# Kernel tuning notes

Measured on AMD Instinct MI355X. Metric: run time of the kernel, lower is better.

The kernel has to match this reference:

```python
import jax, jax.numpy as jnp
import numpy as np

N1 = 200000          # total nodes in batched data1
B = 8                # graphs in data1 (equal-sized)
NPG = N1 // B        # nodes per graph = 25000
N2 = 199             # total nodes in data2 (forced by fc1 in_features 9950 = 50*199)
K = 50               # SortAggregation k
E1 = 2000000
E2 = 3184
F_IN = 128
LN_EPS = 1e-5


def _lin(x, W, b):
    return x @ W + b


def _gin(x, ei, W1a, b1a, W1b, b1b, W2a, b2a, W2b, b2b):
    # GINConv with eps=0: nn((1+eps)*x + sum_{j in N(i)} x_j); messages flow ei[0] -> ei[1]
    agg = jnp.zeros_like(x).at[ei[1]].add(x[ei[0]])
    h = _lin(jax.nn.relu(_lin(x + agg, W1a, b1a)), W1b, b1b)
    h = jax.nn.relu(h)
    agg = jnp.zeros_like(h).at[ei[1]].add(h[ei[0]])
    h2 = _lin(jax.nn.relu(_lin(h + agg, W2a, b2a)), W2b, b2b)
    return jax.nn.relu(h2)


def _cdist(a, b):
    # torch.cdist p=2: [N1, D] x [N2, D] -> [N1, N2]
    sq = (a * a).sum(-1, keepdims=True) + (b * b).sum(-1)[None, :] - 2.0 * (a @ b.T)
    return jnp.sqrt(jnp.maximum(sq, 0.0))


def _sort_pool(x_dense, k):
    # DGCNN sort pooling: sort nodes per graph by last channel, descending; take top-k
    # x_dense: [B, N, D] (all graphs full, so no fill-value padding needed)
    order = jnp.argsort(-x_dense[:, :, -1], axis=-1)[:, :k]       # [B, k]
    return jnp.take_along_axis(x_dense, order[:, :, None], axis=1)  # [B, k, D]


def _layernorm(x, g, b):
    mu = x.mean(-1, keepdims=True)
    var = ((x - mu) ** 2).mean(-1, keepdims=True)
    return (x - mu) * jax.lax.rsqrt(var + LN_EPS) * g + b


def setup_inputs() -> dict:
    key = jax.random.key(0)
    ks = jax.random.split(key, 32)
    s = 0.05
    inp = {
        "x1": jax.random.normal(ks[0], (N1, F_IN), jnp.float32),
        "edge_index1": jax.random.randint(ks[1], (2, E1), 0, N1, jnp.int64),
        "batch1": jnp.repeat(jnp.arange(B, dtype=jnp.int64), NPG),
        "x2": jax.random.normal(ks[2], (N2, F_IN), jnp.float32),
        "edge_index2": jax.random.randint(ks[3], (2, E2), 0, N2, jnp.int64),
        # GIN conv1 MLP: Linear(128,128), ReLU, Linear(128,128)
        "W1a": jax.random.normal(ks[4], (F_IN, 128), jnp.float32) * s,
        "b1a": jnp.zeros((128,), jnp.float32),
        "W1b": jax.random.normal(ks[5], (128, 128), jnp.float32) * s,
        "b1b": jnp.zeros((128,), jnp.float32),
        # GIN conv2 MLP: Linear(128,64), ReLU, Linear(64,64)
        "W2a": jax.random.normal(ks[6], (128, 64), jnp.float32) * s,
        "b2a": jnp.zeros((64,), jnp.float32),
        "W2b": jax.random.normal(ks[7], (64, 64), jnp.float32) * s,
        "b2b": jnp.zeros((64,), jnp.float32),
        # head
        "fc1_W": jax.random.normal(ks[8], (K * N2, 128), jnp.float32) * 0.01,
        "fc1_b": jnp.zeros((128,), jnp.float32),
        "g1": jnp.ones((128,), jnp.float32),
        "be1": jnp.zeros((128,), jnp.float32),
        "fc2_W": jax.random.normal(ks[9], (128, 64), jnp.float32) * s,
        "fc2_b": jnp.zeros((64,), jnp.float32),
        "g2": jnp.ones((64,), jnp.float32),
        "be2": jnp.zeros((64,), jnp.float32),
        "fc3_W": jax.random.normal(ks[10], (64, 1), jnp.float32) * s,
        "fc3_b": jnp.zeros((1,), jnp.float32),
    }
    return inp


def reference(x1, edge_index1, batch1, x2, edge_index2,
              W1a, b1a, W1b, b1b, W2a, b2a, W2b, b2b,
              fc1_W, fc1_b, g1, be1, fc2_W, fc2_b, g2, be2, fc3_W, fc3_b):
    out1 = _gin(x1, edge_index1, W1a, b1a, W1b, b1b, W2a, b2a, W2b, b2b)  # [N1, 64]
    out2 = _gin(x2, edge_index2, W1a, b1a, W1b, b1b, W2a, b2a, W2b, b2b)  # [N2, 64]
    d = _cdist(out1, out2)                       # [N1, N2]
    # graphs in data1 are equal-sized (batch1 = repeat(arange(B), NPG)) -> dense batch is a reshape
    dense = d.reshape(B, NPG, N2)
    pooled = _sort_pool(dense, K).reshape(B, K * N2)  # [B, 9950]
    h = jax.nn.relu(_layernorm(_lin(pooled, fc1_W, fc1_b), g1, be1))
    h = jax.nn.relu(_layernorm(_lin(h, fc2_W, fc2_b), g2, be2))
    return jax.nn.sigmoid(_lin(h, fc3_W, fc3_b))  # [B, 1]
```

## Files before the change

kernel.cpp:

```cpp
#include <hip/hip_runtime.h>
#include <math.h>


#define CPB 64
#define FKS 64

__global__ __launch_bounds__(256) void hist_kernel(const int* __restrict__ dst, int E,
                                                   int* __restrict__ counts) {
    int e = blockIdx.x * 256 + threadIdx.x;
    if (e < E) atomicAdd(&counts[dst[e]], 1);
}

__global__ __launch_bounds__(256) void chunksum_kernel(const int* __restrict__ in, int total,
                                                       int* __restrict__ bsum) {
    __shared__ int red[256];
    int t = threadIdx.x;
    int base = blockIdx.x * 1024 + t * 4;
    int s = 0;
#pragma unroll
    for (int j = 0; j < 4; ++j) { int i = base + j; if (i < total) s += in[i]; }
    red[t] = s; __syncthreads();
    for (int off = 128; off; off >>= 1) { if (t < off) red[t] += red[t + off]; __syncthreads(); }
    if (t == 0) bsum[blockIdx.x] = red[0];
}

__global__ __launch_bounds__(256) void scanchunk_kernel(const int* __restrict__ in, int total,
                                                        const int* __restrict__ baseArr,
                                                        int* __restrict__ out,
                                                        int* __restrict__ out2) {
    __shared__ int tsum[256];
    int t = threadIdx.x;
    int base_i = blockIdx.x * 1024 + t * 4;
    int v[4];
#pragma unroll
    for (int j = 0; j < 4; ++j) v[j] = (base_i + j < total) ? in[base_i + j] : 0;
    int l0 = 0, l1 = v[0], l2 = v[0] + v[1], l3 = l2 + v[2];
    int s = l3 + v[3];
    tsum[t] = s; __syncthreads();
    for (int off = 1; off < 256; off <<= 1) {
        int x = (t >= off) ? tsum[t - off] : 0;
        __syncthreads();
        tsum[t] += x;
        __syncthreads();
    }
    int cb = baseArr ? baseArr[blockIdx.x] : 0;
    int te = cb + tsum[t] - s;
    int outs[4] = { te + l0, te + l1, te + l2, te + l3 };
#pragma unroll
    for (int j = 0; j < 4; ++j) {
        int i = base_i + j;
        if (i < total) { out[i] = outs[j]; if (out2) out2[i] = outs[j]; }
    }
}

__global__ __launch_bounds__(256) void fill_kernel(const int* __restrict__ src,
                                                   const int* __restrict__ dst, int E,
                                                   int* __restrict__ cur, int* __restrict__ csr) {
    int e = blockIdx.x * 256 + threadIdx.x;
    if (e < E) {
        int d = dst[e];
        int p = atomicAdd(&cur[d], 1);
        csr[p] = src[e];
    }
}

template <int KI, int KO, bool BIAS, bool RELU>
__global__ __launch_bounds__(256) void gemm_kernel(const float* __restrict__ X,
                                                   const float* __restrict__ Wm,
                                                   const float* __restrict__ bias,
                                                   float* __restrict__ Y, int N) {
    constexpr int TPR = KO / 4;
    constexpr int RPT = KO / 16;
    constexpr int XS = 68;
    __shared__ __align__(16) float wl[32 * KO];
    __shared__ __align__(16) float xt[32 * XS];
    const int t = threadIdx.x;
    const int r0 = blockIdx.x * 64;
    const int tx = t % TPR, ty = t / TPR;
    float4 acc[RPT];
#pragma unroll
    for (int r = 0; r < RPT; ++r) acc[r] = make_float4(0.f, 0.f, 0.f, 0.f);

    for (int kb = 0; kb < KI; kb += 32) {
        __syncthreads();
#pragma unroll
        for (int i = t; i < 32 * KO / 4; i += 256)
            ((float4*)wl)[i] = ((const float4*)Wm)[kb * KO / 4 + i];
#pragma unroll
        for (int L = t; L < 512; L += 256) {
            int row = L >> 3, kq = L & 7;
            int gr = r0 + row;
            float4 v = make_float4(0.f, 0.f, 0.f, 0.f);
            if (gr < N) v = *(const float4*)(X + (size_t)gr * KI + kb + kq * 4);
            xt[(kq * 4 + 0) * XS + row] = v.x;
            xt[(kq * 4 + 1) * XS + row] = v.y;
            xt[(kq * 4 + 2) * XS + row] = v.z;
            xt[(kq * 4 + 3) * XS + row] = v.w;
        }
        __syncthreads();
#pragma unroll
        for (int k = 0; k < 32; ++k) {
            float4 wv = ((const float4*)wl)[k * TPR + tx];
            const float4* xp = (const float4*)(xt + k * XS + ty * RPT);
#pragma unroll
            for (int rq = 0; rq < RPT / 4; ++rq) {
                float4 xv = xp[rq];
                acc[rq*4+0].x += xv.x * wv.x; acc[rq*4+0].y += xv.x * wv.y;
                acc[rq*4+0].z += xv.x * wv.z; acc[rq*4+0].w += xv.x * wv.w;
                acc[rq*4+1].x += xv.y * wv.x; acc[rq*4+1].y += xv.y * wv.y;
                acc[rq*4+1].z += xv.y * wv.z; acc[rq*4+1].w += xv.y * wv.w;
                acc[rq*4+2].x += xv.z * wv.x; acc[rq*4+2].y += xv.z * wv.y;
                acc[rq*4+2].z += xv.z * wv.z; acc[rq*4+2].w += xv.z * wv.w;
                acc[rq*4+3].x += xv.w * wv.x; acc[rq*4+3].y += xv.w * wv.y;
                acc[rq*4+3].z += xv.w * wv.z; acc[rq*4+3].w += xv.w * wv.w;
            }
        }
    }
    float4 b4 = make_float4(0.f, 0.f, 0.f, 0.f);
    if (BIAS) b4 = ((const float4*)bias)[tx];
#pragma unroll
    for (int r = 0; r < RPT; ++r) {
        int gr = r0 + ty * RPT + r;
        if (gr < N) {
            float4 o = make_float4(acc[r].x + b4.x, acc[r].y + b4.y,
                                   acc[r].z + b4.z, acc[r].w + b4.w);
            if (RELU) {
                o.x = fmaxf(o.x, 0.f); o.y = fmaxf(o.y, 0.f);
                o.z = fmaxf(o.z, 0.f); o.w = fmaxf(o.w, 0.f);
            }
            *(float4*)(Y + (size_t)gr * KO + tx * 4) = o;
        }
    }
}

__global__ __launch_bounds__(256) void gemm23_kernel(const float* __restrict__ X,
                                                     const float* __restrict__ W1,
                                                     const float* __restrict__ b1,
                                                     const float* __restrict__ W2,
                                                     float* __restrict__ Y, int N) {
    __shared__ __align__(16) float wl[32 * 64];
    __shared__ __align__(16) float xt[16 * 68];
    __shared__ __align__(16) float ht[128 * 68];
    const int t = threadIdx.x;
    const int r0 = blockIdx.x * 64;

    const int tx = t & 31, ty = t >> 5;
    float acc[2][16];
#pragma unroll
    for (int r = 0; r < 2; ++r)
#pragma unroll
        for (int c = 0; c < 16; ++c) acc[r][c] = 0.f;

    for (int kb = 0; kb < 128; kb += 16) {
        __syncthreads();
#pragma unroll
        for (int i = t; i < 512; i += 256)
            ((float4*)wl)[i] = ((const float4*)W1)[kb * 32 + i];
        {
            int row = t >> 2, kq = t & 3;
            int gr = r0 + row;
            float4 v = make_float4(0.f, 0.f, 0.f, 0.f);
            if (gr < N) v = *(const float4*)(X + (size_t)gr * 128 + kb + kq * 4);
            xt[(kq * 4 + 0) * 68 + row] = v.x;
            xt[(kq * 4 + 1) * 68 + row] = v.y;
            xt[(kq * 4 + 2) * 68 + row] = v.z;
            xt[(kq * 4 + 3) * 68 + row] = v.w;
        }
        __syncthreads();
#pragma unroll
        for (int kk = 0; kk < 16; ++kk) {
            float2 xv = *(const float2*)(xt + kk * 68 + tx * 2);
            const float4* wp = (const float4*)(wl + kk * 128 + ty * 16);
#pragma unroll
            for (int cq = 0; cq < 4; ++cq) {
                float4 wv = wp[cq];
                acc[0][cq*4+0] += xv.x * wv.x; acc[0][cq*4+1] += xv.x * wv.y;
                acc[0][cq*4+2] += xv.x * wv.z; acc[0][cq*4+3] += xv.x * wv.w;
                acc[1][cq*4+0] += xv.y * wv.x; acc[1][cq*4+1] += xv.y * wv.y;
                acc[1][cq*4+2] += xv.y * wv.z; acc[1][cq*4+3] += xv.y * wv.w;
            }
        }
    }
    {
#pragma unroll
        for (int cq = 0; cq < 4; ++cq) {
            float4 b4 = ((const float4*)b1)[ty * 4 + cq];
            float bb[4] = { b4.x, b4.y, b4.z, b4.w };
#pragma unroll
            for (int j = 0; j < 4; ++j) {
                int col = ty * 16 + cq * 4 + j;
                float2 o;
                o.x = fmaxf(acc[0][cq*4+j] + bb[j], 0.f);
                o.y = fmaxf(acc[1][cq*4+j] + bb[j], 0.f);
                *(float2*)(ht + col * 68 + tx * 2) = o;
            }
        }
    }
    const int tx2 = t & 15, ty2 = t >> 4;
    float4 acc2[4];
#pragma unroll
    for (int r = 0; r < 4; ++r) acc2[r] = make_float4(0.f, 0.f, 0.f, 0.f);
    for (int kb = 0; kb < 4; ++kb) {
        __syncthreads();
#pragma unroll
        for (int i = t; i < 512; i += 256)
            ((float4*)wl)[i] = ((const float4*)W2)[kb * 512 + i];
        __syncthreads();
#pragma unroll
        for (int k = 0; k < 32; ++k) {
            float4 wv = ((const float4*)wl)[k * 16 + tx2];
            float4 xv = *(const float4*)(ht + (kb * 32 + k) * 68 + ty2 * 4);
            acc2[0].x += xv.x * wv.x; acc2[0].y += xv.x * wv.y;
            acc2[0].z += xv.x * wv.z; acc2[0].w += xv.x * wv.w;
            acc2[1].x += xv.y * wv.x; acc2[1].y += xv.y * wv.y;
            acc2[1].z += xv.y * wv.z; acc2[1].w += xv.y * wv.w;
            acc2[2].x += xv.z * wv.x; acc2[2].y += xv.z * wv.y;
            acc2[2].z += xv.z * wv.z; acc2[2].w += xv.z * wv.w;
            acc2[3].x += xv.w * wv.x; acc2[3].y += xv.w * wv.y;
            acc2[3].z += xv.w * wv.z; acc2[3].w += xv.w * wv.w;
        }
    }
#pragma unroll
    for (int r = 0; r < 4; ++r) {
        int gr = r0 + ty2 * 4 + r;
        if (gr < N) *(float4*)(Y + (size_t)gr * 64 + tx2 * 4) = acc2[r];
    }
}

template <int VEC>
__global__ __launch_bounds__(256) void agg_kernel(const float* __restrict__ x,
                                                  const int* __restrict__ rs,
                                                  const int* __restrict__ csr,
                                                  const float* __restrict__ bias,
                                                  float* __restrict__ out, int N) {
    const int NPB = 256 / VEC;
    const int t = threadIdx.x;
    const int node = blockIdx.x * NPB + t / VEC;
    const int c = t % VEC;
    if (node >= N) return;
    const float4* xb = (const float4*)x;
    float4 a0 = xb[(size_t)node * VEC + c];
    float4 a1 = make_float4(0.f, 0.f, 0.f, 0.f);
    int k = rs[node];
    const int s1 = rs[node + 1];
    for (; k + 4 <= s1; k += 4) {
        int i0 = csr[k], i1 = csr[k + 1], i2 = csr[k + 2], i3 = csr[k + 3];
        float4 v0 = xb[(size_t)i0 * VEC + c];
        float4 v1 = xb[(size_t)i1 * VEC + c];
        float4 v2 = xb[(size_t)i2 * VEC + c];
        float4 v3 = xb[(size_t)i3 * VEC + c];
        a0.x += v0.x; a0.y += v0.y; a0.z += v0.z; a0.w += v0.w;
        a1.x += v1.x; a1.y += v1.y; a1.z += v1.z; a1.w += v1.w;
        a0.x += v2.x; a0.y += v2.y; a0.z += v2.z; a0.w += v2.w;
        a1.x += v3.x; a1.y += v3.y; a1.z += v3.z; a1.w += v3.w;
    }
    for (; k < s1; ++k) {
        int i = csr[k];
        float4 v = xb[(size_t)i * VEC + c];
        a0.x += v.x; a0.y += v.y; a0.z += v.z; a0.w += v.w;
    }
    float4 b4 = ((const float4*)bias)[c];
    float4 o;
    o.x = fmaxf(a0.x + a1.x + b4.x, 0.f);
    o.y = fmaxf(a0.y + a1.y + b4.y, 0.f);
    o.z = fmaxf(a0.z + a1.z + b4.z, 0.f);
    o.w = fmaxf(a0.w + a1.w + b4.w, 0.f);
    ((float4*)out)[(size_t)node * VEC + c] = o;
}

__global__ __launch_bounds__(256) void scores_kernel(const float* __restrict__ out1,
                                                     const float* __restrict__ out2,
                                                     double* __restrict__ sc, int N) {
    const int t = threadIdx.x;
    const int node = blockIdx.x * 4 + (t >> 6);
    const int lane = t & 63;
    if (node >= N) return;
    float a = out1[(size_t)node * 64 + lane];
    float bv = out2[198 * 64 + lane];
    double na = (double)a * a;
    double nb = (double)bv * bv;
    double dd = (double)a * bv;
    for (int off = 32; off; off >>= 1) {
        na += __shfl_xor(na, off);
        nb += __shfl_xor(nb, off);
        dd += __shfl_xor(dd, off);
    }
    if (lane == 0) {
        double sq = na + nb - 2.0 * dd;
        sc[node] = (sq > 0.0) ? sqrt(sq) : 0.0;
    }
}

__global__ __launch_bounds__(256) void topkA_kernel(const double* __restrict__ sc,
                                                    double* __restrict__ cv,
                                                    int* __restrict__ ci, int npg) {
    const int g = blockIdx.x / CPB, cb = blockIdx.x % CPB;
    const int chunk = (npg + CPB - 1) / CPB;
    const int base = cb * chunk;
    const int len = (npg - base < chunk) ? (npg - base) : chunk;
    const int t = threadIdx.x;
    __shared__ double lv[400];
    __shared__ double wvs[4];
    __shared__ int wss[4];
    const double* s = sc + (size_t)g * npg;
    for (int i = t; i < chunk; i += 256)
        lv[i] = (i < len) ? s[base + i] : -1.0e300;
    __syncthreads();
    const int ob = (g * CPB + cb) * 50;
    for (int r = 0; r < 50; ++r) {
        double bv = -1.0e300; int bs = 0x3fffffff;
        for (int i = t; i < chunk; i += 256) {
            double v = lv[i];
            if (v > bv || (v == bv && i < bs)) { bv = v; bs = i; }
        }
#pragma unroll
        for (int off = 32; off; off >>= 1) {
            double ov = __shfl_xor(bv, off);
            int os = __shfl_xor(bs, off);
            if (ov > bv || (ov == bv && os < bs)) { bv = ov; bs = os; }
        }
        if ((t & 63) == 0) { wvs[t >> 6] = bv; wss[t >> 6] = bs; }
        __syncthreads();
        if (t == 0) {
#pragma unroll
            for (int w = 1; w < 4; ++w)
                if (wvs[w] > bv || (wvs[w] == bv && wss[w] < bs)) { bv = wvs[w]; bs = wss[w]; }
            cv[ob + r] = bv;
            ci[ob + r] = base + bs;
            lv[bs] = -1.0e300;
        }
        __syncthreads();
    }
}

__global__ __launch_bounds__(256) void topkB_kernel(const double* __restrict__ cv,
                                                    const int* __restrict__ ci,
                                                    int* __restrict__ topk) {
    const int g = blockIdx.x, t = threadIdx.x;
    const int M = CPB * 50;
    __shared__ double lv[CPB * 50];
    __shared__ int li[CPB * 50];
    __shared__ double wvs[4];
    __shared__ int wis[4], wss[4];
    for (int i = t; i < M; i += 256) {
        lv[i] = cv[(size_t)g * M + i];
        li[i] = ci[(size_t)g * M + i];
    }
    __syncthreads();
    for (int r = 0; r < 50; ++r) {
        double bv = -1.0e300; int bi = 0x3fffffff, bs = 0;
        for (int i = t; i < M; i += 256) {
            double v = lv[i]; int idx = li[i];
            if (v > bv || (v == bv && idx < bi)) { bv = v; bi = idx; bs = i; }
        }
#pragma unroll
        for (int off = 32; off; off >>= 1) {
            double ov = __shfl_xor(bv, off);
            int oi = __shfl_xor(bi, off);
            int os = __shfl_xor(bs, off);
            if (ov > bv || (ov == bv && oi < bi)) { bv = ov; bi = oi; bs = os; }
        }
        if ((t & 63) == 0) { wvs[t >> 6] = bv; wis[t >> 6] = bi; wss[t >> 6] = bs; }
        __syncthreads();
        if (t == 0) {
#pragma unroll
            for (int w = 1; w < 4; ++w)
                if (wvs[w] > bv || (wvs[w] == bv && wis[w] < bi)) {
                    bv = wvs[w]; bi = wis[w]; bs = wss[w];
                }
            topk[g * 50 + r] = bi;
            lv[bs] = -1.0e300;
        }
        __syncthreads();
    }
}

__global__ __launch_bounds__(256) void pooled_kernel(const float* __restrict__ out1,
                                                     const float* __restrict__ out2,
                                                     const int* __restrict__ topk,
                                                     float* __restrict__ pooled, int npg) {
    const int bk = blockIdx.x;
    const int g = bk / 50, kk = bk % 50;
    __shared__ float arow[64];
    const int t = threadIdx.x;
    const int node = g * npg + topk[g * 50 + kk];
    if (t < 64) arow[t] = out1[(size_t)node * 64 + t];
    __syncthreads();
    if (t < 199) {
        double na = 0.0, nb = 0.0, dd = 0.0;
        for (int k2 = 0; k2 < 64; ++k2) {
            double a = arow[k2];
            double b = out2[t * 64 + k2];
            na += a * a; nb += b * b; dd += a * b;
        }
        double sq = na + nb - 2.0 * dd;
        pooled[(size_t)g * 9950 + kk * 199 + t] = (float)((sq > 0.0) ? sqrt(sq) : 0.0);
    }
}

__global__ __launch_bounds__(256) void fc1_partial_kernel(const float* __restrict__ pooled,
                                                          const float* __restrict__ W,
                                                          double* __restrict__ part) {
    const int b = blockIdx.x >> 6;
    const int ks = blockIdx.x & (FKS - 1);
    const int t = threadIdx.x;
    const int f = t & 127, half = t >> 7;
    const int C = (9950 + FKS - 1) / FKS;
    const int i0 = ks * C;
    const int i1 = (i0 + C < 9950) ? (i0 + C) : 9950;
    const float* p = pooled + (size_t)b * 9950;
    double acc = 0.0;
    for (int i = i0 + half; i < i1; i += 2)
        acc += (double)p[i] * (double)W[(size_t)i * 128 + f];
    __shared__ double red[256];
    red[t] = acc; __syncthreads();
    if (half == 0)
        part[((size_t)b * FKS + ks) * 128 + f] = red[f] + red[128 + f];
}

__global__ __launch_bounds__(128) void fc1_reduce_kernel(const double* __restrict__ part,
                                                         const float* __restrict__ bias,
                                                         float* __restrict__ z1) {
    const int b = blockIdx.x, f = threadIdx.x;
    double acc = 0.0;
    for (int ks = 0; ks < FKS; ++ks)
        acc += part[((size_t)b * FKS + ks) * 128 + f];
    z1[b * 128 + f] = (float)(acc + (double)bias[f]);
}

__global__ __launch_bounds__(128) void head_kernel(const float* __restrict__ z1,
                                                   const float* __restrict__ g1,
                                                   const float* __restrict__ be1,
                                                   const float* __restrict__ W2,
                                                   const float* __restrict__ b2,
                                                   const float* __restrict__ g2,
                                                   const float* __restrict__ be2,
                                                   const float* __restrict__ W3,
                                                   const float* __restrict__ b3,
                                                   float* __restrict__ out) {
    const int b = blockIdx.x, t = threadIdx.x;
    __shared__ double red[128];
    __shared__ float shy[128];
    __shared__ float sh2[64];
    float z = z1[b * 128 + t];
    red[t] = z; __syncthreads();
    for (int off = 64; off; off >>= 1) { if (t < off) red[t] += red[t + off]; __syncthreads(); }
    double mu = red[0] / 128.0; __syncthreads();
    double dv = (double)z - mu;
    red[t] = dv * dv; __syncthreads();
    for (int off = 64; off; off >>= 1) { if (t < off) red[t] += red[t + off]; __syncthreads(); }
    double var = red[0] / 128.0; __syncthreads();
    float y = (float)(dv / sqrt(var + 1e-5)) * g1[t] + be1[t];
    shy[t] = fmaxf(y, 0.f); __syncthreads();
    double a2 = 0.0;
    if (t < 64) {
        for (int i = 0; i < 128; ++i) a2 += (double)shy[i] * (double)W2[i * 64 + t];
        a2 += (double)b2[t];
    }
    red[t] = (t < 64) ? a2 : 0.0; __syncthreads();
    for (int off = 64; off; off >>= 1) { if (t < off) red[t] += red[t + off]; __syncthreads(); }
    double mu2 = red[0] / 64.0; __syncthreads();
    double dv2 = a2 - mu2;
    red[t] = (t < 64) ? dv2 * dv2 : 0.0; __syncthreads();
    for (int off = 64; off; off >>= 1) { if (t < off) red[t] += red[t + off]; __syncthreads(); }
    double var2 = red[0] / 64.0; __syncthreads();
    if (t < 64) {
        float h2 = (float)(dv2 / sqrt(var2 + 1e-5)) * g2[t] + be2[t];
        sh2[t] = fmaxf(h2, 0.f);
    }
    __syncthreads();
    red[t] = (t < 64) ? (double)sh2[t] * (double)W3[t] : 0.0; __syncthreads();
    for (int off = 64; off; off >>= 1) { if (t < off) red[t] += red[t + off]; __syncthreads(); }
    if (t == 0) {
        double zf = red[0] + (double)b3[0];
        out[b] = (float)(1.0 / (1.0 + exp(-zf)));
    }
}

extern "C" void kernel_launch(void* const* d_in, const int* in_sizes, int n_in,
                              void* d_out, int out_size, void* d_ws, size_t ws_size,
                              hipStream_t stream) {
    (void)n_in; (void)out_size; (void)ws_size;
    const float* x1  = (const float*)d_in[0];
    const int*   ei1 = (const int*)d_in[1];
    const float* x2  = (const float*)d_in[3];
    const int*   ei2 = (const int*)d_in[4];
    const float* W1a = (const float*)d_in[5];
    const float* b1a = (const float*)d_in[6];
    const float* W1b = (const float*)d_in[7];
    const float* b1b = (const float*)d_in[8];
    const float* W2a = (const float*)d_in[9];
    const float* b2a = (const float*)d_in[10];
    const float* W2b = (const float*)d_in[11];
    const float* b2b = (const float*)d_in[12];
    const float* f1W = (const float*)d_in[13];
    const float* f1b = (const float*)d_in[14];
    const float* g1  = (const float*)d_in[15];
    const float* be1 = (const float*)d_in[16];
    const float* f2W = (const float*)d_in[17];
    const float* f2b = (const float*)d_in[18];
    const float* g2  = (const float*)d_in[19];
    const float* be2 = (const float*)d_in[20];
    const float* f3W = (const float*)d_in[21];
    const float* f3b = (const float*)d_in[22];
    float* out = (float*)d_out;

    const int n1 = in_sizes[0] / 128;
    const int e1 = in_sizes[1] / 2;
    const int n2 = in_sizes[3] / 128;
    const int e2 = in_sizes[4] / 2;
    const int npg = n1 / 8;

    char* p = (char*)d_ws;
    auto alloc = [&](size_t bytes) { char* r = p; p += (bytes + 255) & ~(size_t)255; return r; };
    float*  A    = (float*)alloc((size_t)n1 * 128 * 4);
    float*  Bb   = (float*)alloc((size_t)n1 * 128 * 4);
    double* sc   = (double*)alloc((size_t)n1 * 8);
    int*    rs1  = (int*)alloc((size_t)(n1 + 1) * 4);
    int*    cur1 = (int*)alloc((size_t)(n1 + 1) * 4);
    int*    csr1 = (int*)alloc((size_t)e1 * 4);
    int*    bsum = (int*)alloc(4096);
    int*    rs2  = (int*)alloc((size_t)(n2 + 1) * 4);
    int*    cur2 = (int*)alloc((size_t)(n2 + 1) * 4);
    int*    csr2 = (int*)alloc((size_t)e2 * 4);
    float*  G2A  = (float*)alloc((size_t)n2 * 128 * 4);
    float*  G2B  = (float*)alloc((size_t)n2 * 128 * 4);
    float*  o2   = (float*)alloc((size_t)n2 * 64 * 4);
    double* cndv = (double*)alloc((size_t)8 * CPB * 50 * 8);
    int*    cndi = (int*)alloc((size_t)8 * CPB * 50 * 4);
    int*    tk   = (int*)alloc(8 * 50 * 4);
    float*  pld  = (float*)alloc((size_t)8 * 9950 * 4);
    double* f1p  = (double*)alloc((size_t)8 * FKS * 128 * 8);
    float*  z1   = (float*)alloc(8 * 128 * 4);

    const int* src1 = ei1;           const int* dst1 = ei1 + e1;
    const int* src2 = ei2;           const int* dst2 = ei2 + e2;

    hipMemsetAsync(rs1, 0, (size_t)(n1 + 1) * 4, stream);
    hipMemsetAsync(rs2, 0, (size_t)(n2 + 1) * 4, stream);
    hist_kernel<<<(e1 + 255) / 256, 256, 0, stream>>>(dst1, e1, rs1);
    hist_kernel<<<(e2 + 255) / 256, 256, 0, stream>>>(dst2, e2, rs2);
    int tot1 = n1 + 1, nch1 = (tot1 + 1023) / 1024;
    chunksum_kernel<<<nch1, 256, 0, stream>>>(rs1, tot1, bsum);
    scanchunk_kernel<<<1, 256, 0, stream>>>(bsum, nch1, nullptr, bsum, nullptr);
    scanchunk_kernel<<<nch1, 256, 0, stream>>>(rs1, tot1, bsum, rs1, cur1);
    fill_kernel<<<(e1 + 255) / 256, 256, 0, stream>>>(src1, dst1, e1, cur1, csr1);
    int tot2 = n2 + 1, nch2 = (tot2 + 1023) / 1024;
    chunksum_kernel<<<nch2, 256, 0, stream>>>(rs2, tot2, bsum);
    scanchunk_kernel<<<1, 256, 0, stream>>>(bsum, nch2, nullptr, bsum, nullptr);
    scanchunk_kernel<<<nch2, 256, 0, stream>>>(rs2, tot2, bsum, rs2, cur2);
    fill_kernel<<<(e2 + 255) / 256, 256, 0, stream>>>(src2, dst2, e2, cur2, csr2);

    int gb1 = (n1 + 63) / 64;
    gemm_kernel<128, 128, false, false><<<gb1, 256, 0, stream>>>(x1, W1a, nullptr, A, n1);
    agg_kernel<32><<<(n1 + 7) / 8, 256, 0, stream>>>(A, rs1, csr1, b1a, Bb, n1);
    gemm23_kernel<<<gb1, 256, 0, stream>>>(Bb, W1b, b1b, W2a, A, n1);
    agg_kernel<16><<<(n1 + 15) / 16, 256, 0, stream>>>(A, rs1, csr1, b2a, Bb, n1);
    gemm_kernel<64, 64, true, true><<<gb1, 256, 0, stream>>>(Bb, W2b, b2b, A, n1);

    int gb2 = (n2 + 63) / 64;
    gemm_kernel<128, 128, false, false><<<gb2, 256, 0, stream>>>(x2, W1a, nullptr, G2A, n2);
    agg_kernel<32><<<(n2 + 7) / 8, 256, 0, stream>>>(G2A, rs2, csr2, b1a, G2B, n2);
    gemm23_kernel<<<gb2, 256, 0, stream>>>(G2B, W1b, b1b, W2a, G2A, n2);
    agg_kernel<16><<<(n2 + 15) / 16, 256, 0, stream>>>(G2A, rs2, csr2, b2a, G2B, n2);
    gemm_kernel<64, 64, true, true><<<gb2, 256, 0, stream>>>(G2B, W2b, b2b, o2, n2);

    scores_kernel<<<(n1 + 3) / 4, 256, 0, stream>>>(A, o2, sc, n1);
    topkA_kernel<<<8 * CPB, 256, 0, stream>>>(sc, cndv, cndi, npg);
    topkB_kernel<<<8, 256, 0, stream>>>(cndv, cndi, tk);
    pooled_kernel<<<400, 256, 0, stream>>>(A, o2, tk, pld, npg);

    fc1_partial_kernel<<<8 * FKS, 256, 0, stream>>>(pld, f1W, f1p);
    fc1_reduce_kernel<<<8, 128, 0, stream>>>(f1p, f1b, z1);
    head_kernel<<<8, 128, 0, stream>>>(z1, g1, be1, f2W, f2b, g2, be2, f3W, f3b, out);
}
```

Baseline: 1.334 ms.

## Batch both graphs into one CSR, halve gemm23 LDS, unroll aggregation by eight

Places the two graphs into a single combined node and edge space with offset indices, so each GIN stage runs as one launch over both graphs instead of two. gemm23 now stages the hidden tile in two 64-column halves, which cuts its shared memory roughly in half and should allow more resident blocks. The aggregation gather loop is unrolled to eight neighbours so more loads are in flight. The batching removes several small launches and a separate scan pass, at the cost of extra barriers in gemm23.

```diff
diff --git a/kernel.cpp b/kernel.cpp
--- a/kernel.cpp
+++ b/kernel.cpp
@@ -6,9 +6,9 @@
 #define FKS 64
 
 __global__ __launch_bounds__(256) void hist_kernel(const int* __restrict__ dst, int E,
-                                                   int* __restrict__ counts) {
+                                                   int* __restrict__ counts, int base) {
     int e = blockIdx.x * 256 + threadIdx.x;
-    if (e < E) atomicAdd(&counts[dst[e]], 1);
+    if (e < E) atomicAdd(&counts[dst[e] + base], 1);
 }
 
 __global__ __launch_bounds__(256) void chunksum_kernel(const int* __restrict__ in, int total,
@@ -55,12 +55,13 @@
 
 __global__ __launch_bounds__(256) void fill_kernel(const int* __restrict__ src,
                                                    const int* __restrict__ dst, int E,
-                                                   int* __restrict__ cur, int* __restrict__ csr) {
+                                                   int* __restrict__ cur, int* __restrict__ csr,
+                                                   int base) {
     int e = blockIdx.x * 256 + threadIdx.x;
     if (e < E) {
-        int d = dst[e];
+        int d = dst[e] + base;
         int p = atomicAdd(&cur[d], 1);
-        csr[p] = src[e];
+        csr[p] = src[e] + base;
     }
 }
 
@@ -140,7 +141,7 @@
                                                      float* __restrict__ Y, int N) {
     __shared__ __align__(16) float wl[32 * 64];
     __shared__ __align__(16) float xt[16 * 68];
-    __shared__ __align__(16) float ht[128 * 68];
+    __shared__ __align__(16) float ht[64 * 66];
     const int t = threadIdx.x;
     const int r0 = blockIdx.x * 64;
 
@@ -181,43 +182,48 @@
             }
         }
     }
-    {
-#pragma unroll
-        for (int cq = 0; cq < 4; ++cq) {
-            float4 b4 = ((const float4*)b1)[ty * 4 + cq];
-            float bb[4] = { b4.x, b4.y, b4.z, b4.w };
-#pragma unroll
-            for (int j = 0; j < 4; ++j) {
-                int col = ty * 16 + cq * 4 + j;
-                float2 o;
-                o.x = fmaxf(acc[0][cq*4+j] + bb[j], 0.f);
-                o.y = fmaxf(acc[1][cq*4+j] + bb[j], 0.f);
-                *(float2*)(ht + col * 68 + tx * 2) = o;
-            }
-        }
-    }
+
     const int tx2 = t & 15, ty2 = t >> 4;
     float4 acc2[4];
 #pragma unroll
     for (int r = 0; r < 4; ++r) acc2[r] = make_float4(0.f, 0.f, 0.f, 0.f);
-    for (int kb = 0; kb < 4; ++kb) {
-        __syncthreads();
-#pragma unroll
-        for (int i = t; i < 512; i += 256)
-            ((float4*)wl)[i] = ((const float4*)W2)[kb * 512 + i];
-        __syncthreads();
-#pragma unroll
-        for (int k = 0; k < 32; ++k) {
-            float4 wv = ((const float4*)wl)[k * 16 + tx2];
-            float4 xv = *(const float4*)(ht + (kb * 32 + k) * 68 + ty2 * 4);
-            acc2[0].x += xv.x * wv.x; acc2[0].y += xv.x * wv.y;
-            acc2[0].z += xv.x * wv.z; acc2[0].w += xv.x * wv.w;
-            acc2[1].x += xv.y * wv.x; acc2[1].y += xv.y * wv.y;
-            acc2[1].z += xv.y * wv.z; acc2[1].w += xv.y * wv.w;
-            acc2[2].x += xv.z * wv.x; acc2[2].y += xv.z * wv.y;
-            acc2[2].z += xv.z * wv.z; acc2[2].w += xv.z * wv.w;
-            acc2[3].x += xv.w * wv.x; acc2[3].y += xv.w * wv.y;
-            acc2[3].z += xv.w * wv.z; acc2[3].w += xv.w * wv.w;
+
+    for (int half = 0; half < 2; ++half) {
+        __syncthreads();
+        if ((ty >> 2) == half) {
+#pragma unroll
+            for (int cq = 0; cq < 4; ++cq) {
+                float4 b4 = ((const float4*)b1)[ty * 4 + cq];
+                float bb[4] = { b4.x, b4.y, b4.z, b4.w };
+#pragma unroll
+                for (int j = 0; j < 4; ++j) {
+                    int col_local = (ty & 3) * 16 + cq * 4 + j;
+                    float2 o;
+                    o.x = fmaxf(acc[0][cq*4+j] + bb[j], 0.f);
+                    o.y = fmaxf(acc[1][cq*4+j] + bb[j], 0.f);
+                    *(float2*)(ht + col_local * 66 + tx * 2) = o;
+                }
+            }
+        }
+        for (int kb = 0; kb < 2; ++kb) {
+            __syncthreads();
+#pragma unroll
+            for (int i = t; i < 512; i += 256)
+                ((float4*)wl)[i] = ((const float4*)W2)[(half * 64 + kb * 32) * 16 + i];
+            __syncthreads();
+#pragma unroll
+            for (int k = 0; k < 32; ++k) {
+                float4 wv = ((const float4*)wl)[k * 16 + tx2];
+                float4 xv = *(const float4*)(ht + (kb * 32 + k) * 66 + ty2 * 4);
+                acc2[0].x += xv.x * wv.x; acc2[0].y += xv.x * wv.y;
+                acc2[0].z += xv.x * wv.z; acc2[0].w += xv.x * wv.w;
+                acc2[1].x += xv.y * wv.x; acc2[1].y += xv.y * wv.y;
+                acc2[1].z += xv.y * wv.z; acc2[1].w += xv.y * wv.w;
+                acc2[2].x += xv.z * wv.x; acc2[2].y += xv.z * wv.y;
+                acc2[2].z += xv.z * wv.z; acc2[2].w += xv.z * wv.w;
+                acc2[3].x += xv.w * wv.x; acc2[3].y += xv.w * wv.y;
+                acc2[3].z += xv.w * wv.z; acc2[3].w += xv.w * wv.w;
+            }
         }
     }
 #pragma unroll
@@ -243,8 +249,28 @@
     float4 a1 = make_float4(0.f, 0.f, 0.f, 0.f);
     int k = rs[node];
     const int s1 = rs[node + 1];
-    for (; k + 4 <= s1; k += 4) {
-        int i0 = csr[k], i1 = csr[k + 1], i2 = csr[k + 2], i3 = csr[k + 3];
+    for (; k + 8 <= s1; k += 8) {
+        int i0 = csr[k], i1 = csr[k+1], i2 = csr[k+2], i3 = csr[k+3];
+        int i4 = csr[k+4], i5 = csr[k+5], i6 = csr[k+6], i7 = csr[k+7];
+        float4 v0 = xb[(size_t)i0 * VEC + c];
+        float4 v1 = xb[(size_t)i1 * VEC + c];
+        float4 v2 = xb[(size_t)i2 * VEC + c];
+        float4 v3 = xb[(size_t)i3 * VEC + c];
+        float4 v4 = xb[(size_t)i4 * VEC + c];
+        float4 v5 = xb[(size_t)i5 * VEC + c];
+        float4 v6 = xb[(size_t)i6 * VEC + c];
+        float4 v7 = xb[(size_t)i7 * VEC + c];
+        a0.x += v0.x; a0.y += v0.y; a0.z += v0.z; a0.w += v0.w;
+        a1.x += v1.x; a1.y += v1.y; a1.z += v1.z; a1.w += v1.w;
+        a0.x += v2.x; a0.y += v2.y; a0.z += v2.z; a0.w += v2.w;
+        a1.x += v3.x; a1.y += v3.y; a1.z += v3.z; a1.w += v3.w;
+        a0.x += v4.x; a0.y += v4.y; a0.z += v4.z; a0.w += v4.w;
+        a1.x += v5.x; a1.y += v5.y; a1.z += v5.z; a1.w += v5.w;
+        a0.x += v6.x; a0.y += v6.y; a0.z += v6.z; a0.w += v6.w;
+        a1.x += v7.x; a1.y += v7.y; a1.z += v7.z; a1.w += v7.w;
+    }
+    if (k + 4 <= s1) {
+        int i0 = csr[k], i1 = csr[k+1], i2 = csr[k+2], i3 = csr[k+3];
         float4 v0 = xb[(size_t)i0 * VEC + c];
         float4 v1 = xb[(size_t)i1 * VEC + c];
         float4 v2 = xb[(size_t)i2 * VEC + c];
@@ -253,6 +279,7 @@
         a1.x += v1.x; a1.y += v1.y; a1.z += v1.z; a1.w += v1.w;
         a0.x += v2.x; a0.y += v2.y; a0.z += v2.z; a0.w += v2.w;
         a1.x += v3.x; a1.y += v3.y; a1.z += v3.z; a1.w += v3.w;
+        k += 4;
     }
     for (; k < s1; ++k) {
         int i = csr[k];
@@ -510,22 +537,18 @@
     const int n2 = in_sizes[3] / 128;
     const int e2 = in_sizes[4] / 2;
     const int npg = n1 / 8;
+    const int n  = n1 + n2;
+    const int et = e1 + e2;
 
     char* p = (char*)d_ws;
     auto alloc = [&](size_t bytes) { char* r = p; p += (bytes + 255) & ~(size_t)255; return r; };
-    float*  A    = (float*)alloc((size_t)n1 * 128 * 4);
-    float*  Bb   = (float*)alloc((size_t)n1 * 128 * 4);
+    float*  A    = (float*)alloc((size_t)n * 128 * 4);
+    float*  Bb   = (float*)alloc((size_t)n * 128 * 4);
     double* sc   = (double*)alloc((size_t)n1 * 8);
-    int*    rs1  = (int*)alloc((size_t)(n1 + 1) * 4);
-    int*    cur1 = (int*)alloc((size_t)(n1 + 1) * 4);
-    int*    csr1 = (int*)alloc((size_t)e1 * 4);
+    int*    rs   = (int*)alloc((size_t)(n + 1) * 4);
+    int*    cur  = (int*)alloc((size_t)(n + 1) * 4);
+    int*    csr  = (int*)alloc((size_t)et * 4);
     int*    bsum = (int*)alloc(4096);
-    int*    rs2  = (int*)alloc((size_t)(n2 + 1) * 4);
-    int*    cur2 = (int*)alloc((size_t)(n2 + 1) * 4);
-    int*    csr2 = (int*)alloc((size_t)e2 * 4);
-    float*  G2A  = (float*)alloc((size_t)n2 * 128 * 4);
-    float*  G2B  = (float*)alloc((size_t)n2 * 128 * 4);
-    float*  o2   = (float*)alloc((size_t)n2 * 64 * 4);
     double* cndv = (double*)alloc((size_t)8 * CPB * 50 * 8);
     int*    cndi = (int*)alloc((size_t)8 * CPB * 50 * 4);
     int*    tk   = (int*)alloc(8 * 50 * 4);
@@ -536,39 +559,34 @@
     const int* src1 = ei1;           const int* dst1 = ei1 + e1;
     const int* src2 = ei2;           const int* dst2 = ei2 + e2;
 
-    hipMemsetAsync(rs1, 0, (size_t)(n1 + 1) * 4, stream);
-    hipMemsetAsync(rs2, 0, (size_t)(n2 + 1) * 4, stream);
-    hist_kernel<<<(e1 + 255) / 256, 256, 0, stream>>>(dst1, e1, rs1);
-    hist_kernel<<<(e2 + 255) / 256, 256, 0, stream>>>(dst2, e2, rs2);
-    int tot1 = n1 + 1, nch1 = (tot1 + 1023) / 1024;
-    chunksum_kernel<<<nch1, 256, 0, stream>>>(rs1, tot1, bsum);
-    scanchunk_kernel<<<1, 256, 0, stream>>>(bsum, nch1, nullptr, bsum, nullptr);
-    scanchunk_kernel<<<nch1, 256, 0, stream>>>(rs1, tot1, bsum, rs1, cur1);
-    fill_kernel<<<(e1 + 255) / 256, 256, 0, stream>>>(src1, dst1, e1, cur1, csr1);
-    int tot2 = n2 + 1, nch2 = (tot2 + 1023) / 1024;
-    chunksum_kernel<<<nch2, 256, 0, stream>>>(rs2, tot2, bsum);
-    scanchunk_kernel<<<1, 256, 0, stream>>>(bsum, nch2, nullptr, bsum, nullptr);
-    scanchunk_kernel<<<nch2, 256, 0, stream>>>(rs2, tot2, bsum, rs2, cur2);
-    fill_kernel<<<(e2 + 255) / 256, 256, 0, stream>>>(src2, dst2, e2, cur2, csr2);
-
+    hipMemsetAsync(rs, 0, (size_t)(n + 1) * 4, stream);
+    hist_kernel<<<(e1 + 255) / 256, 256, 0, stream>>>(dst1, e1, rs, 0);
+    hist_kernel<<<(e2 + 255) / 256, 256, 0, stream>>>(dst2, e2, rs, n1);
+    int tot = n + 1, nch = (tot + 1023) / 1024;
+    chunksum_kernel<<<nch, 256, 0, stream>>>(rs, tot, bsum);
+    scanchunk_kernel<<<1, 256, 0, stream>>>(bsum, nch, nullptr, bsum, nullptr);
+    scanchunk_kernel<<<nch, 256, 0, stream>>>(rs, tot, bsum, rs, cur);
+    fill_kernel<<<(e1 + 255) / 256, 256, 0, stream>>>(src1, dst1, e1, cur, csr, 0);
+    fill_kernel<<<(e2 + 255) / 256, 256, 0, stream>>>(src2, dst2, e2, cur, csr, n1);
+
+    int gb  = (n + 63) / 64;
     int gb1 = (n1 + 63) / 64;
+    int gb2 = (n2 + 63) / 64;
     gemm_kernel<128, 128, false, false><<<gb1, 256, 0, stream>>>(x1, W1a, nullptr, A, n1);
-    agg_kernel<32><<<(n1 + 7) / 8, 256, 0, stream>>>(A, rs1, csr1, b1a, Bb, n1);
-    gemm23_kernel<<<gb1, 256, 0, stream>>>(Bb, W1b, b1b, W2a, A, n1);
-    agg_kernel<16><<<(n1 + 15) / 16, 256, 0, stream>>>(A, rs1, csr1, b2a, Bb, n1);
-    gemm_kernel<64, 64, true, true><<<gb1, 256, 0, stream>>>(Bb, W2b, b2b, A, n1);
-
-    int gb2 = (n2 + 63) / 64;
-    gemm_kernel<128, 128, false, false><<<gb2, 256, 0, stream>>>(x2, W1a, nullptr, G2A, n2);
-    agg_kernel<32><<<(n2 + 7) / 8, 256, 0, stream>>>(G2A, rs2, csr2, b1a, G2B, n2);
-    gemm23_kernel<<<gb2, 256, 0, stream>>>(G2B, W1b, b1b, W2a, G2A, n2);
-    agg_kernel<16><<<(n2 + 15) / 16, 256, 0, stream>>>(G2A, rs2, csr2, b2a, G2B, n2);
-    gemm_kernel<64, 64, true, true><<<gb2, 256, 0, stream>>>(G2B, W2b, b2b, o2, n2);
-
-    scores_kernel<<<(n1 + 3) / 4, 256, 0, stream>>>(A, o2, sc, n1);
+    gemm_kernel<128, 128, false, false><<<gb2, 256, 0, stream>>>(x2, W1a, nullptr,
+                                                                 A + (size_t)n1 * 128, n2);
+    agg_kernel<32><<<(n + 7) / 8, 256, 0, stream>>>(A, rs, csr, b1a, Bb, n);
+    gemm23_kernel<<<gb, 256, 0, stream>>>(Bb, W1b, b1b, W2a, A, n);
+    agg_kernel<16><<<(n + 15) / 16, 256, 0, stream>>>(A, rs, csr, b2a, Bb, n);
+    gemm_kernel<64, 64, true, true><<<gb, 256, 0, stream>>>(Bb, W2b, b2b, A, n);
+
+    const float* out1 = A;
+    const float* o2   = A + (size_t)n1 * 64;
+
+    scores_kernel<<<(n1 + 3) / 4, 256, 0, stream>>>(out1, o2, sc, n1);
     topkA_kernel<<<8 * CPB, 256, 0, stream>>>(sc, cndv, cndi, npg);
     topkB_kernel<<<8, 256, 0, stream>>>(cndv, cndi, tk);
-    pooled_kernel<<<400, 256, 0, stream>>>(A, o2, tk, pld, npg);
+    pooled_kernel<<<400, 256, 0, stream>>>(out1, o2, tk, pld, npg);
 
     fc1_partial_kernel<<<8 * FKS, 256, 0, stream>>>(pld, f1W, f1p);
     fc1_reduce_kernel<<<8, 128, 0, stream>>>(f1p, f1b, z1);
```

Result: slower. 1.368 ms (+2.5%).
